# Kernel optimization log

Measured on AMD Instinct MI355X. Metric: run time of the kernel, lower is better.

The kernel has to match this reference:

```python
import jax, jax.numpy as jnp
import numpy as np
from functools import partial

U = 1200   # thought_size (GRU units)
E = 620    # word_size
V = 20000  # vocab_size
B = 128    # batch
T = 64     # seq_len
LN_EPS = 1e-3  # Keras LayerNormalization default epsilon


def layernorm(x, gamma, beta, eps=LN_EPS):
    m = jnp.mean(x, axis=-1, keepdims=True)
    v = jnp.mean(jnp.square(x - m), axis=-1, keepdims=True)
    return gamma * (x - m) * jax.lax.rsqrt(v + eps) + beta


def gru_ln_direction(emb, kernel, rkernel, bias, ln0_g, ln0_b, ln3_g, ln3_b):
    """Run the LayerNorm-GRU (impl=2, reset_after=True) over emb [B,T,E].
    Returns final hidden state [B,U]."""
    input_bias, recurrent_bias = bias[0], bias[1]
    # Time-parallel input projection: [B,T,3U]
    x_proj = jnp.einsum('bte,eu->btu', emb, kernel) + input_bias
    x_proj_t = jnp.transpose(x_proj, (1, 0, 2))  # [T,B,3U]

    def step(h, xt):
        h_ln = layernorm(h, ln0_g, ln0_b)                      # LN on previous state
        inner = h_ln @ rkernel + recurrent_bias                # [B,3U]
        z = jax.nn.sigmoid(xt[:, :U] + inner[:, :U])
        r = jax.nn.sigmoid(xt[:, U:2 * U] + inner[:, U:2 * U])
        rec_h = r * inner[:, 2 * U:]
        hh = jnp.tanh(layernorm(xt[:, 2 * U:] + rec_h, ln3_g, ln3_b))
        h_new = z * h_ln + (1.0 - z) * hh
        return h_new, None

    h0 = jnp.zeros((emb.shape[0], U), dtype=emb.dtype)
    h_final, _ = jax.lax.scan(step, h0, x_proj_t)
    return h_final


def setup_inputs() -> dict:
    key = jax.random.key(0)
    ks = jax.random.split(key, 8)
    s = 0.05
    return {
        'sentences': jax.random.randint(ks[0], (B, T), 0, V),
        'embed': jax.random.normal(ks[1], (V, E), jnp.float32) * s,
        'fw_kernel': jax.random.normal(ks[2], (E, 3 * U), jnp.float32) * s,
        'fw_rkernel': jax.random.normal(ks[3], (U, 3 * U), jnp.float32) * s,
        'fw_bias': jax.random.normal(ks[4], (2, 3 * U), jnp.float32) * s,
        'fw_ln0_g': jnp.ones((U,), jnp.float32),
        'fw_ln0_b': jnp.zeros((U,), jnp.float32),
        'fw_ln3_g': jnp.ones((U,), jnp.float32),
        'fw_ln3_b': jnp.zeros((U,), jnp.float32),
        'bw_kernel': jax.random.normal(ks[5], (E, 3 * U), jnp.float32) * s,
        'bw_rkernel': jax.random.normal(ks[6], (U, 3 * U), jnp.float32) * s,
        'bw_bias': jax.random.normal(ks[7], (2, 3 * U), jnp.float32) * s,
        'bw_ln0_g': jnp.ones((U,), jnp.float32),
        'bw_ln0_b': jnp.zeros((U,), jnp.float32),
        'bw_ln3_g': jnp.ones((U,), jnp.float32),
        'bw_ln3_b': jnp.zeros((U,), jnp.float32),
    }


def reference(sentences, embed, fw_kernel, fw_rkernel, fw_bias,
              fw_ln0_g, fw_ln0_b, fw_ln3_g, fw_ln3_b,
              bw_kernel, bw_rkernel, bw_bias,
              bw_ln0_g, bw_ln0_b, bw_ln3_g, bw_ln3_b):
    embedding = jnp.tanh(embed[sentences])  # [B,T,E]
    forward_h = gru_ln_direction(embedding, fw_kernel, fw_rkernel, fw_bias,
                                 fw_ln0_g, fw_ln0_b, fw_ln3_g, fw_ln3_b)
    backward_h = gru_ln_direction(embedding[:, ::-1, :], bw_kernel, bw_rkernel, bw_bias,
                                  bw_ln0_g, bw_ln0_b, bw_ln3_g, bw_ln3_b)
    thought_vector = jnp.concatenate([forward_h, backward_h], axis=1)  # [B,2U]
    return thought_vector, embedding
```

## Files before the change

kernel.cpp:

```cpp
#include <hip/hip_runtime.h>
#include <hip/hip_bf16.h>

#define U_    1200
#define E_    620
#define B_    128
#define T_    64
#define N3    3600
#define NP    3712
#define KE    640
#define KU    1216
#define WIN   16
#define LN_EPS 1e-3f

#define GBLK  232
#define UBLK  128
#define TBLK  (GBLK + UBLK)

typedef __attribute__((ext_vector_type(8))) short short8;
typedef __attribute__((ext_vector_type(4))) float f32x4;
typedef _Float16 f16;
typedef __attribute__((ext_vector_type(8))) _Float16 half8;

constexpr size_t OFF_EMBH  = 0;
constexpr size_t SZ_EMB    = (size_t)8192 * KE * 2;
constexpr size_t OFF_EMBL  = OFF_EMBH + SZ_EMB;
constexpr size_t OFF_KTH   = OFF_EMBL + SZ_EMB;
constexpr size_t SZ_KT     = (size_t)2 * NP * KE * 2;
constexpr size_t OFF_KTL   = OFF_KTH + SZ_KT;
constexpr size_t OFF_RKF   = OFF_KTL + SZ_KT;
constexpr size_t SZ_RKF    = (size_t)2 * NP * KU * 2;
constexpr size_t OFF_XPW   = OFF_RKF + SZ_RKF;
constexpr size_t SZ_XPW    = (size_t)2 * WIN * B_ * NP * 4;
constexpr size_t OFF_INNER = OFF_XPW + SZ_XPW;
constexpr size_t SZ_INNER  = (size_t)4 * B_ * NP * 4;
constexpr size_t OFF_HLN   = OFF_INNER + SZ_INNER;
constexpr size_t SZ_HLN    = (size_t)2 * B_ * U_ * 4;
constexpr size_t OFF_HLFH  = OFF_HLN + SZ_HLN;
constexpr size_t SZ_HLF    = (size_t)2 * B_ * KU * 2;
constexpr size_t OFF_HLFL  = OFF_HLFH + SZ_HLF;

__device__ inline void lds_load16(const void* g, void* l) {
  __builtin_amdgcn_global_load_lds(
      (const __attribute__((address_space(1))) unsigned int*)g,
      (__attribute__((address_space(3))) unsigned int*)l, 16, 0, 0);
}

__device__ inline float sigmf(float x) { return 1.f / (1.f + expf(-x)); }

__device__ inline int swz_scol(int tid) {
  return (((tid & 7) ^ ((tid >> 3) & 7)) << 3);
}
__device__ inline int swz_off(int row, int kk, int lane) {
  return row * 64 + ((kk * 32 + ((lane >> 4) << 3)) ^ ((row & 7) << 3));
}

__global__ __launch_bounds__(256)
void embed_kernel(const int* __restrict__ sent, const float* __restrict__ embed,
                  float* __restrict__ out_emb,
                  __hip_bfloat16* __restrict__ embH, __hip_bfloat16* __restrict__ embL) {
  const int row = blockIdx.x;
  const int idx = sent[row];
  const float* src = embed + (size_t)idx * E_;
  for (int e = threadIdx.x; e < KE; e += 256) {
    float v = 0.f;
    if (e < E_) {
      v = tanhf(src[e]);
      out_emb[(size_t)row * E_ + e] = v;
    }
    const __hip_bfloat16 hi = __float2bfloat16(v);
    embH[(size_t)row * KE + e] = hi;
    embL[(size_t)row * KE + e] = __float2bfloat16(v - __bfloat162float(hi));
  }
}

__global__ __launch_bounds__(256)
void transpose_cast(const float* __restrict__ W0, const float* __restrict__ W1,
                    __hip_bfloat16* __restrict__ WtHi, __hip_bfloat16* __restrict__ WtLo,
                    int Kreal, int Kp) {
  const int d = blockIdx.z;
  const float* W = d ? W1 : W0;
  __hip_bfloat16* dstH = WtHi + (size_t)d * NP * Kp;
  __hip_bfloat16* dstL = WtLo + (size_t)d * NP * Kp;
  __shared__ float tile[32][33];
  const int n0 = blockIdx.x * 32, k0 = blockIdx.y * 32;
  const int tx = threadIdx.x, ty = threadIdx.y;
#pragma unroll
  for (int i = 0; i < 32; i += 8) {
    const int k = k0 + ty + i, n = n0 + tx;
    tile[ty + i][tx] = (k < Kreal && n < N3) ? W[(size_t)k * N3 + n] : 0.f;
  }
  __syncthreads();
#pragma unroll
  for (int i = 0; i < 32; i += 8) {
    const int n = n0 + ty + i, k = k0 + tx;
    const float v = tile[tx][ty + i];
    const __hip_bfloat16 hi = __float2bfloat16(v);
    dstH[(size_t)n * Kp + k] = hi;
    dstL[(size_t)n * Kp + k] = __float2bfloat16(v - __bfloat162float(hi));
  }
}

__global__ __launch_bounds__(256)
void transpose_cast_f16(const float* __restrict__ W0, const float* __restrict__ W1,
                        f16* __restrict__ Wt, int Kreal, int Kp) {
  const int d = blockIdx.z;
  const float* W = d ? W1 : W0;
  f16* dst = Wt + (size_t)d * NP * Kp;
  __shared__ float tile[32][33];
  const int n0 = blockIdx.x * 32, k0 = blockIdx.y * 32;
  const int tx = threadIdx.x, ty = threadIdx.y;
#pragma unroll
  for (int i = 0; i < 32; i += 8) {
    const int k = k0 + ty + i, n = n0 + tx;
    tile[ty + i][tx] = (k < Kreal && n < N3) ? W[(size_t)k * N3 + n] : 0.f;
  }
  __syncthreads();
#pragma unroll
  for (int i = 0; i < 32; i += 8) {
    const int n = n0 + ty + i, k = k0 + tx;
    dst[(size_t)n * Kp + k] = (f16)tile[tx][ty + i];
  }
}

__global__ __launch_bounds__(256)
void init_hln(const float* __restrict__ fw_b0, const float* __restrict__ bw_b0,
              float* __restrict__ hln, f16* __restrict__ hlfH, f16* __restrict__ hlfL) {
  const int idx = blockIdx.x * 256 + threadIdx.x;
  if (idx >= 2 * B_ * KU) return;
  const int k = idx % KU;
  const int rowd = idx / KU;
  const int d = rowd >> 7;
  float v = 0.f;
  if (k < U_) {
    v = (d ? bw_b0 : fw_b0)[k];
    hln[(size_t)rowd * U_ + k] = v;
  }
  const f16 hi = (f16)v;
  hlfH[idx] = hi;
  hlfL[idx] = (f16)(v - (float)hi);
}

__global__ __launch_bounds__(256)
void xwin_gemm(const __hip_bfloat16* __restrict__ embH, const __hip_bfloat16* __restrict__ embL,
               const __hip_bfloat16* __restrict__ kTH, const __hip_bfloat16* __restrict__ kTL,
               const float* __restrict__ fw_bias, const float* __restrict__ bw_bias,
               float* __restrict__ xpw, int w0) {
  constexpr int BM = 128, BN = 128, BK = 64;
  constexpr int WM = 64, WN = 64, FM = 4, FN = 4;
  const int bid = blockIdx.x;
  const int w = (bid & 7) * 116 + (bid >> 3);
  const int d = w / 464;
  const int q = w % 464;
  const int nt = q / 16, mt = q % 16;
  const int m0 = mt * BM;
  const int n0 = nt * BN;

  const __hip_bfloat16* BH = kTH + (size_t)d * NP * KE;
  const __hip_bfloat16* BL = kTL + (size_t)d * NP * KE;

  const int tid = threadIdx.x;
  const int lane = tid & 63;
  const int wid = tid >> 6;
  const int wr = wid >> 1, wc = wid & 1;

  __shared__ __align__(16) __hip_bfloat16 xs[65536];

  f32x4 acc[FM][FN] = {};

  const int srow = tid >> 3;
  const int scol = swz_scol(tid);

#define XSTG(buf_, ks_)                                                        \
  {                                                                            \
    const int k0s = (ks_) * BK;                                                \
    __hip_bfloat16* base = xs + (buf_) * 32768;                                \
    _Pragma("unroll")                                                          \
    for (int it = 0; it < 4; ++it) {                                           \
      const int row = m0 + it * 32 + srow;                                     \
      const int b = row & 127, sr = row >> 7;                                  \
      const int txi = d ? (T_ - 1 - (w0 + sr)) : (w0 + sr);                    \
      const size_t goff = (size_t)(b * T_ + txi) * KE + k0s + scol;            \
      lds_load16(embH + goff, base + it * 2048 + tid * 8);                     \
      lds_load16(embL + goff, base + 8192 + it * 2048 + tid * 8);              \
    }                                                                          \
    _Pragma("unroll")                                                          \
    for (int it = 0; it < 4; ++it) {                                           \
      const size_t goff = (size_t)(n0 + it * 32 + srow) * KE + k0s + scol;     \
      lds_load16(BH + goff, base + 16384 + it * 2048 + tid * 8);               \
      lds_load16(BL + goff, base + 24576 + it * 2048 + tid * 8);               \
    }                                                                          \
  }

  XSTG(0, 0)
  __syncthreads();
  int cur = 0;
  for (int ks = 0; ks < KE / BK; ++ks) {
    if (ks + 1 < KE / BK) XSTG(cur ^ 1, ks + 1)
    const __hip_bfloat16* AH = xs + cur * 32768;
    const __hip_bfloat16* AL = AH + 8192;
    const __hip_bfloat16* BHs = AH + 16384;
    const __hip_bfloat16* BLs = AH + 24576;
#pragma unroll
    for (int kk = 0; kk < 2; ++kk) {
      short8 ah[FM], al[FM], bh[FN], bl[FN];
#pragma unroll
      for (int mi = 0; mi < FM; ++mi) {
        const int row = wr * WM + mi * 16 + (lane & 15);
        const int off = swz_off(row, kk, lane);
        ah[mi] = *(const short8*)(AH + off);
        al[mi] = *(const short8*)(AL + off);
      }
#pragma unroll
      for (int ni = 0; ni < FN; ++ni) {
        const int row = wc * WN + ni * 16 + (lane & 15);
        const int off = swz_off(row, kk, lane);
        bh[ni] = *(const short8*)(BHs + off);
        bl[ni] = *(const short8*)(BLs + off);
      }
#pragma unroll
      for (int mi = 0; mi < FM; ++mi)
#pragma unroll
        for (int ni = 0; ni < FN; ++ni) {
          acc[mi][ni] = __builtin_amdgcn_mfma_f32_16x16x32_bf16(ah[mi], bh[ni], acc[mi][ni], 0, 0, 0);
          acc[mi][ni] = __builtin_amdgcn_mfma_f32_16x16x32_bf16(ah[mi], bl[ni], acc[mi][ni], 0, 0, 0);
          acc[mi][ni] = __builtin_amdgcn_mfma_f32_16x16x32_bf16(al[mi], bh[ni], acc[mi][ni], 0, 0, 0);
        }
    }
    __syncthreads();
    cur ^= 1;
  }
#undef XSTG

  const float* ib = d ? bw_bias : fw_bias;
#pragma unroll
  for (int mi = 0; mi < FM; ++mi)
#pragma unroll
    for (int ni = 0; ni < FN; ++ni) {
      const int gc = n0 + wc * WN + ni * 16 + (lane & 15);
      const float bv = (gc < N3) ? ib[gc] : 0.f;
      const int gr0 = m0 + wr * WM + mi * 16 + ((lane >> 4) << 2);
#pragma unroll
      for (int j = 0; j < 4; ++j) {
        const int gr = gr0 + j;
        const int b = gr & 127, srel = gr >> 7;
        const size_t off = ((size_t)(d * WIN + srel) * B_ + b) * NP + gc;
        xpw[off] = acc[mi][ni][j] + bv;
      }
    }
}

__device__ inline void breduce2(float& a, float& b, float* red, int tid) {
#pragma unroll
  for (int off = 32; off; off >>= 1) {
    a += __shfl_down(a, off, 64);
    b += __shfl_down(b, off, 64);
  }
  const int w = tid >> 6;
  __syncthreads();
  if ((tid & 63) == 0) { red[w] = a; red[4 + w] = b; }
  __syncthreads();
  a = red[0] + red[1] + red[2] + red[3];
  b = red[4] + red[5] + red[6] + red[7];
}

__global__ __launch_bounds__(256)
void step_fused(const f16* __restrict__ rkF,
                f16* __restrict__ hlfH, f16* __restrict__ hlfL,
                float* __restrict__ hln, float* __restrict__ inner,
                const float* __restrict__ xpw,
                const float* __restrict__ fw_bias, const float* __restrict__ bw_bias,
                const float* __restrict__ fw_ln0g, const float* __restrict__ fw_ln0b,
                const float* __restrict__ fw_ln3g, const float* __restrict__ fw_ln3b,
                const float* __restrict__ bw_ln0g, const float* __restrict__ bw_ln0b,
                const float* __restrict__ bw_ln3g, const float* __restrict__ bw_ln3b,
                float* __restrict__ out_tv,
                int dG, int doG, int dU, int tU, int doU) {
  __shared__ __align__(16) f16 smem[24576];
  __shared__ float red[8];

  const int bid = blockIdx.x;
  const int tid = threadIdx.x;

  if (bid < GBLK) {
    if (!doG) return;
    const int x  = bid & 7;
    const int kp = x >> 2;
    const int nh = (x >> 1) & 1;
    const int m  = x & 1;
    const int i  = bid >> 3;
    const int nt = i + 29 * nh;
    const int ks0 = kp ? 10 : 0;
    const int ks1 = kp ? 19 : 10;
    const int m0 = m * 64;
    const int n0 = nt * 64;

    const int lane = tid & 63;
    const int wid = tid >> 6;
    const int wr = wid >> 1, wc = wid & 1;

    const f16* WF = rkF + (size_t)dG * NP * KU;

    f32x4 acc[2][2] = {};
    const int srow = tid >> 3;
    const int scol = swz_scol(tid);

#define STG(buf_, ks_)                                                         \
  {                                                                            \
    const int k0s = (ks_) * 64;                                                \
    f16* base = smem + (buf_) * 12288;                                         \
    _Pragma("unroll")                                                          \
    for (int it = 0; it < 2; ++it) {                                           \
      const size_t ga = (size_t)(dG * B_ + m0 + it * 32 + srow) * KU + k0s + scol; \
      lds_load16(hlfH + ga, base + it * 2048 + tid * 8);                       \
      lds_load16(hlfL + ga, base + 4096 + it * 2048 + tid * 8);                \
      const size_t gb = (size_t)(n0 + it * 32 + srow) * KU + k0s + scol;       \
      lds_load16(WF + gb, base + 8192 + it * 2048 + tid * 8);                  \
    }                                                                          \
  }

    STG(0, ks0)
    __syncthreads();
    int cur = 0;
    for (int ks = ks0; ks < ks1; ++ks) {
      if (ks + 1 < ks1) STG(cur ^ 1, ks + 1)
      const f16* AH = smem + cur * 12288;
      const f16* AL = AH + 4096;
      const f16* BW = AH + 8192;
#pragma unroll
      for (int kk = 0; kk < 2; ++kk) {
        half8 ah[2], al[2], bv[2];
#pragma unroll
        for (int mi = 0; mi < 2; ++mi) {
          const int row = wr * 32 + mi * 16 + (lane & 15);
          const int off = swz_off(row, kk, lane);
          ah[mi] = *(const half8*)(AH + off);
          al[mi] = *(const half8*)(AL + off);
        }
#pragma unroll
        for (int nf = 0; nf < 2; ++nf) {
          const int row = wc * 32 + nf * 16 + (lane & 15);
          const int off = swz_off(row, kk, lane);
          bv[nf] = *(const half8*)(BW + off);
        }
#pragma unroll
        for (int mi = 0; mi < 2; ++mi)
#pragma unroll
          for (int nf = 0; nf < 2; ++nf) {
            acc[mi][nf] = __builtin_amdgcn_mfma_f32_16x16x32_f16(ah[mi], bv[nf], acc[mi][nf], 0, 0, 0);
            acc[mi][nf] = __builtin_amdgcn_mfma_f32_16x16x32_f16(al[mi], bv[nf], acc[mi][nf], 0, 0, 0);
          }
      }
      __syncthreads();
      cur ^= 1;
    }
#undef STG

    float* C = inner + (size_t)(dG * 2 + kp) * B_ * NP;
#pragma unroll
    for (int mi = 0; mi < 2; ++mi)
#pragma unroll
      for (int nf = 0; nf < 2; ++nf) {
        const int gc = n0 + wc * 32 + nf * 16 + (lane & 15);
        const int gr = m0 + wr * 32 + mi * 16 + ((lane >> 4) << 2);
#pragma unroll
        for (int j = 0; j < 4; ++j)
          C[(size_t)(gr + j) * NP + gc] = acc[mi][nf][j];
      }
    return;
  }

  if (!doU) return;
  const int r = bid - GBLK;
  const int d = dU;
  const int srel = tU & (WIN - 1);

  const float* rec0 = inner + ((size_t)(d * 2 + 0) * B_ + r) * NP;
  const float* rec1 = inner + ((size_t)(d * 2 + 1) * B_ + r) * NP;
  const float* xr = xpw + ((size_t)(d * WIN + srel) * B_ + r) * NP;
  const float* rb = (d ? bw_bias : fw_bias) + N3;
  const float* g0 = d ? bw_ln0g : fw_ln0g;
  const float* b0 = d ? bw_ln0b : fw_ln0b;
  const float* g3 = d ? bw_ln3g : fw_ln3g;
  const float* b3 = d ? bw_ln3b : fw_ln3b;
  float* hl = hln + ((size_t)d * B_ + r) * U_;
  f16* hlbH = hlfH + ((size_t)d * B_ + r) * KU;
  f16* hlbL = hlfL + ((size_t)d * B_ + r) * KU;

  float zv[5], cv[5], hv[5];
  float s1 = 0.f, s2 = 0.f;
#pragma unroll
  for (int i = 0; i < 5; ++i) {
    const int c = tid + i * 256;
    if (c < U_) {
      const float z  = sigmf(xr[c] + rec0[c] + rec1[c] + rb[c]);
      const float rr = sigmf(xr[U_ + c] + rec0[U_ + c] + rec1[U_ + c] + rb[U_ + c]);
      const float cand = xr[2 * U_ + c] +
                         rr * (rec0[2 * U_ + c] + rec1[2 * U_ + c] + rb[2 * U_ + c]);
      zv[i] = z; cv[i] = cand;
      s1 += cand; s2 += cand * cand;
    }
  }
  breduce2(s1, s2, red, tid);
  const float m1 = s1 / U_;
  const float is1 = rsqrtf(s2 / U_ - m1 * m1 + LN_EPS);

  float t1 = 0.f, t2 = 0.f;
#pragma unroll
  for (int i = 0; i < 5; ++i) {
    const int c = tid + i * 256;
    if (c < U_) {
      const float hh = tanhf(g3[c] * (cv[i] - m1) * is1 + b3[c]);
      const float hn = zv[i] * hl[c] + (1.f - zv[i]) * hh;
      hv[i] = hn;
      t1 += hn; t2 += hn * hn;
    }
  }
  breduce2(t1, t2, red, tid);
  const float m2 = t1 / U_;
  const float is2 = rsqrtf(t2 / U_ - m2 * m2 + LN_EPS);

#pragma unroll
  for (int i = 0; i < 5; ++i) {
    const int c = tid + i * 256;
    if (c < U_) {
      const float hlnew = g0[c] * (hv[i] - m2) * is2 + b0[c];
      hl[c] = hlnew;
      const f16 hi = (f16)hlnew;
      hlbH[c] = hi;
      hlbL[c] = (f16)(hlnew - (float)hi);
      if (tU == T_ - 1) out_tv[(size_t)r * 2400 + (size_t)d * U_ + c] = hv[i];
    }
  }
}

extern "C" void kernel_launch(void* const* d_in, const int* in_sizes, int n_in,
                              void* d_out, int out_size, void* d_ws, size_t ws_size,
                              hipStream_t stream) {
  const int*   sent      = (const int*)  d_in[0];
  const float* embed     = (const float*)d_in[1];
  const float* fw_kernel = (const float*)d_in[2];
  const float* fw_rkern  = (const float*)d_in[3];
  const float* fw_bias   = (const float*)d_in[4];
  const float* fw_ln0g   = (const float*)d_in[5];
  const float* fw_ln0b   = (const float*)d_in[6];
  const float* fw_ln3g   = (const float*)d_in[7];
  const float* fw_ln3b   = (const float*)d_in[8];
  const float* bw_kernel = (const float*)d_in[9];
  const float* bw_rkern  = (const float*)d_in[10];
  const float* bw_bias   = (const float*)d_in[11];
  const float* bw_ln0g   = (const float*)d_in[12];
  const float* bw_ln0b   = (const float*)d_in[13];
  const float* bw_ln3g   = (const float*)d_in[14];
  const float* bw_ln3b   = (const float*)d_in[15];

  uint8_t* ws = (uint8_t*)d_ws;
  __hip_bfloat16* embH  = (__hip_bfloat16*)(ws + OFF_EMBH);
  __hip_bfloat16* embL  = (__hip_bfloat16*)(ws + OFF_EMBL);
  __hip_bfloat16* kTH   = (__hip_bfloat16*)(ws + OFF_KTH);
  __hip_bfloat16* kTL   = (__hip_bfloat16*)(ws + OFF_KTL);
  f16*            rkF   = (f16*)(ws + OFF_RKF);
  float*          xpw   = (float*)(ws + OFF_XPW);
  float*          inner = (float*)(ws + OFF_INNER);
  float*          hln   = (float*)(ws + OFF_HLN);
  f16*            hlfH  = (f16*)(ws + OFF_HLFH);
  f16*            hlfL  = (f16*)(ws + OFF_HLFL);

  float* out_tv  = (float*)d_out;
  float* out_emb = (float*)d_out + (size_t)B_ * 2 * U_;

  embed_kernel<<<B_ * T_, 256, 0, stream>>>(sent, embed, out_emb, embH, embL);

  transpose_cast<<<dim3(NP / 32, KE / 32, 2), dim3(32, 8), 0, stream>>>(
      fw_kernel, bw_kernel, kTH, kTL, E_, KE);
  transpose_cast_f16<<<dim3(NP / 32, KU / 32, 2), dim3(32, 8), 0, stream>>>(
      fw_rkern, bw_rkern, rkF, U_, KU);

  init_hln<<<(2 * B_ * KU + 255) / 256, 256, 0, stream>>>(fw_ln0b, bw_ln0b,
                                                          hln, hlfH, hlfL);

#define SF(dG_, doG_, dU_, tU_, doU_)                                          \
  step_fused<<<TBLK, 256, 0, stream>>>(                                        \
      rkF, hlfH, hlfL, hln, inner, xpw,                                        \
      fw_bias, bw_bias, fw_ln0g, fw_ln0b, fw_ln3g, fw_ln3b,                    \
      bw_ln0g, bw_ln0b, bw_ln3g, bw_ln3b, out_tv,                              \
      dG_, doG_, dU_, tU_, doU_)

  for (int t = 0; t < T_; ++t) {
    SF(0, 1, 1, t - 1, (t > 0) ? 1 : 0);
    if ((t & (WIN - 1)) == 0)
      xwin_gemm<<<928, 256, 0, stream>>>(
          embH, embL, kTH, kTL, fw_bias, bw_bias, xpw, t);
    SF(1, 1, 0, t, 1);
  }
  SF(0, 0, 1, T_ - 1, 1);
#undef SF
}
```

Measured before the change: 1.892 ms.

## Split recurrent GEMM K across four partials and single-buffer the input-projection GEMM

The recurrent GEMM part of the fused step kernel moves from a 2-way to a 4-way K split, doubling the GEMM block count to 464 so more CUs work on each step. The update blocks now sum four partial inner buffers, which adds memory traffic per step. Separately, the windowed input-projection GEMM drops its double-buffered LDS prefetch for a simpler load, sync, compute loop. That halves its LDS footprint and may raise occupancy, but global loads no longer overlap with MFMA work.

```diff
diff --git a/kernel.cpp b/kernel.cpp
--- a/kernel.cpp
+++ b/kernel.cpp
@@ -12,7 +12,7 @@
 #define WIN   16
 #define LN_EPS 1e-3f
 
-#define GBLK  232
+#define GBLK  464
 #define UBLK  128
 #define TBLK  (GBLK + UBLK)
 
@@ -32,7 +32,7 @@
 constexpr size_t OFF_XPW   = OFF_RKF + SZ_RKF;
 constexpr size_t SZ_XPW    = (size_t)2 * WIN * B_ * NP * 4;
 constexpr size_t OFF_INNER = OFF_XPW + SZ_XPW;
-constexpr size_t SZ_INNER  = (size_t)4 * B_ * NP * 4;
+constexpr size_t SZ_INNER  = (size_t)8 * B_ * NP * 4;
 constexpr size_t OFF_HLN   = OFF_INNER + SZ_INNER;
 constexpr size_t SZ_HLN    = (size_t)2 * B_ * U_ * 4;
 constexpr size_t OFF_HLFH  = OFF_HLN + SZ_HLN;
@@ -147,6 +147,7 @@
                float* __restrict__ xpw, int w0) {
   constexpr int BM = 128, BN = 128, BK = 64;
   constexpr int WM = 64, WN = 64, FM = 4, FN = 4;
+  constexpr int TA = BM * BK, TB = BN * BK;
   const int bid = blockIdx.x;
   const int w = (bid & 7) * 116 + (bid >> 3);
   const int d = w / 464;
@@ -163,59 +164,49 @@
   const int wid = tid >> 6;
   const int wr = wid >> 1, wc = wid & 1;
 
-  __shared__ __align__(16) __hip_bfloat16 xs[65536];
+  __shared__ __align__(16) __hip_bfloat16 As[2 * TA];
+  __shared__ __align__(16) __hip_bfloat16 Bs[2 * TB];
 
   f32x4 acc[FM][FN] = {};
 
   const int srow = tid >> 3;
   const int scol = swz_scol(tid);
 
-#define XSTG(buf_, ks_)                                                        \
-  {                                                                            \
-    const int k0s = (ks_) * BK;                                                \
-    __hip_bfloat16* base = xs + (buf_) * 32768;                                \
-    _Pragma("unroll")                                                          \
-    for (int it = 0; it < 4; ++it) {                                           \
-      const int row = m0 + it * 32 + srow;                                     \
-      const int b = row & 127, sr = row >> 7;                                  \
-      const int txi = d ? (T_ - 1 - (w0 + sr)) : (w0 + sr);                    \
-      const size_t goff = (size_t)(b * T_ + txi) * KE + k0s + scol;            \
-      lds_load16(embH + goff, base + it * 2048 + tid * 8);                     \
-      lds_load16(embL + goff, base + 8192 + it * 2048 + tid * 8);              \
-    }                                                                          \
-    _Pragma("unroll")                                                          \
-    for (int it = 0; it < 4; ++it) {                                           \
-      const size_t goff = (size_t)(n0 + it * 32 + srow) * KE + k0s + scol;     \
-      lds_load16(BH + goff, base + 16384 + it * 2048 + tid * 8);               \
-      lds_load16(BL + goff, base + 24576 + it * 2048 + tid * 8);               \
-    }                                                                          \
-  }
-
-  XSTG(0, 0)
-  __syncthreads();
-  int cur = 0;
   for (int ks = 0; ks < KE / BK; ++ks) {
-    if (ks + 1 < KE / BK) XSTG(cur ^ 1, ks + 1)
-    const __hip_bfloat16* AH = xs + cur * 32768;
-    const __hip_bfloat16* AL = AH + 8192;
-    const __hip_bfloat16* BHs = AH + 16384;
-    const __hip_bfloat16* BLs = AH + 24576;
-#pragma unroll
-    for (int kk = 0; kk < 2; ++kk) {
+    const int k0 = ks * BK;
+    __syncthreads();
+#pragma unroll
+    for (int it = 0; it < TA / 2048; ++it) {
+      const int row = m0 + it * 32 + srow;
+      const int b = row & 127, srel = row >> 7;
+      const int txi = d ? (T_ - 1 - (w0 + srel)) : (w0 + srel);
+      const size_t goff = (size_t)(b * T_ + txi) * KE + k0 + scol;
+      lds_load16(embH + goff, As + it * 2048 + tid * 8);
+      lds_load16(embL + goff, As + TA + it * 2048 + tid * 8);
+    }
+#pragma unroll
+    for (int it = 0; it < TB / 2048; ++it) {
+      const size_t goff = (size_t)(n0 + it * 32 + srow) * KE + k0 + scol;
+      lds_load16(BH + goff, Bs + it * 2048 + tid * 8);
+      lds_load16(BL + goff, Bs + TB + it * 2048 + tid * 8);
+    }
+    __syncthreads();
+#pragma unroll
+    for (int kk = 0; kk < BK / 32; ++kk) {
       short8 ah[FM], al[FM], bh[FN], bl[FN];
 #pragma unroll
       for (int mi = 0; mi < FM; ++mi) {
         const int row = wr * WM + mi * 16 + (lane & 15);
         const int off = swz_off(row, kk, lane);
-        ah[mi] = *(const short8*)(AH + off);
-        al[mi] = *(const short8*)(AL + off);
+        ah[mi] = *(const short8*)(As + off);
+        al[mi] = *(const short8*)(As + TA + off);
       }
 #pragma unroll
       for (int ni = 0; ni < FN; ++ni) {
         const int row = wc * WN + ni * 16 + (lane & 15);
         const int off = swz_off(row, kk, lane);
-        bh[ni] = *(const short8*)(BHs + off);
-        bl[ni] = *(const short8*)(BLs + off);
+        bh[ni] = *(const short8*)(Bs + off);
+        bl[ni] = *(const short8*)(Bs + TB + off);
       }
 #pragma unroll
       for (int mi = 0; mi < FM; ++mi)
@@ -226,10 +217,7 @@
           acc[mi][ni] = __builtin_amdgcn_mfma_f32_16x16x32_bf16(al[mi], bh[ni], acc[mi][ni], 0, 0, 0);
         }
     }
-    __syncthreads();
-    cur ^= 1;
-  }
-#undef XSTG
+  }
 
   const float* ib = d ? bw_bias : fw_bias;
 #pragma unroll
@@ -284,13 +272,11 @@
   if (bid < GBLK) {
     if (!doG) return;
     const int x  = bid & 7;
-    const int kp = x >> 2;
-    const int nh = (x >> 1) & 1;
+    const int kp = x >> 1;
     const int m  = x & 1;
-    const int i  = bid >> 3;
-    const int nt = i + 29 * nh;
-    const int ks0 = kp ? 10 : 0;
-    const int ks1 = kp ? 19 : 10;
+    const int nt = bid >> 3;
+    const int ks0 = kp * 5;
+    const int ks1 = (kp == 3) ? 19 : (ks0 + 5);
     const int m0 = m * 64;
     const int n0 = nt * 64;
 
@@ -355,7 +341,7 @@
     }
 #undef STG
 
-    float* C = inner + (size_t)(dG * 2 + kp) * B_ * NP;
+    float* C = inner + (size_t)(dG * 4 + kp) * B_ * NP;
 #pragma unroll
     for (int mi = 0; mi < 2; ++mi)
 #pragma unroll
@@ -374,8 +360,10 @@
   const int d = dU;
   const int srel = tU & (WIN - 1);
 
-  const float* rec0 = inner + ((size_t)(d * 2 + 0) * B_ + r) * NP;
-  const float* rec1 = inner + ((size_t)(d * 2 + 1) * B_ + r) * NP;
+  const float* rec0 = inner + ((size_t)(d * 4 + 0) * B_ + r) * NP;
+  const float* rec1 = inner + ((size_t)(d * 4 + 1) * B_ + r) * NP;
+  const float* rec2 = inner + ((size_t)(d * 4 + 2) * B_ + r) * NP;
+  const float* rec3 = inner + ((size_t)(d * 4 + 3) * B_ + r) * NP;
   const float* xr = xpw + ((size_t)(d * WIN + srel) * B_ + r) * NP;
   const float* rb = (d ? bw_bias : fw_bias) + N3;
   const float* g0 = d ? bw_ln0g : fw_ln0g;
@@ -392,10 +380,12 @@
   for (int i = 0; i < 5; ++i) {
     const int c = tid + i * 256;
     if (c < U_) {
-      const float z  = sigmf(xr[c] + rec0[c] + rec1[c] + rb[c]);
-      const float rr = sigmf(xr[U_ + c] + rec0[U_ + c] + rec1[U_ + c] + rb[U_ + c]);
-      const float cand = xr[2 * U_ + c] +
-                         rr * (rec0[2 * U_ + c] + rec1[2 * U_ + c] + rb[2 * U_ + c]);
+      const float rz = (rec0[c] + rec1[c]) + (rec2[c] + rec3[c]);
+      const float rg = (rec0[U_ + c] + rec1[U_ + c]) + (rec2[U_ + c] + rec3[U_ + c]);
+      const float rh = (rec0[2 * U_ + c] + rec1[2 * U_ + c]) + (rec2[2 * U_ + c] + rec3[2 * U_ + c]);
+      const float z  = sigmf(xr[c] + rz + rb[c]);
+      const float rr = sigmf(xr[U_ + c] + rg + rb[U_ + c]);
+      const float cand = xr[2 * U_ + c] + rr * (rh + rb[2 * U_ + c]);
       zv[i] = z; cv[i] = cand;
       s1 += cand; s2 += cand * cand;
     }
```

New measurement: 1.788 ms, median of 2. 1.06x faster.
